# Performance work log

Hardware: AMD Instinct MI355X
Metric: run time of the kernel (lower is better)

Reference implementation:

```python
import jax, jax.numpy as jnp
import numpy as np
from jax import lax

C = 64
RED = 8
BN_EPS = 1e-5

def _conv1x1(x, W, b):
    # x: [N,C,H,W], W: [O,C] (1x1 conv kernel squeezed), b: [O]
    return jnp.einsum('nchw,oc->nohw', x, W) + b[None, :, None, None]

def _cross_attention(img, depth, Wq, bq, Wk, bk, Wv, bv, gamma):
    # img, depth: [N,C,H,W]; channel-channel attention (attn is [N,C,C])
    N, c, H, Wd = img.shape
    HW = H * Wd
    q = _conv1x1(img, Wq, bq).reshape(N, c, HW).astype(jnp.float32)
    k = _conv1x1(depth, Wk, bk).reshape(N, c, HW).astype(jnp.float32)
    v = _conv1x1(depth, Wv, bv).reshape(N, c, HW).astype(jnp.float32)
    attn = jax.nn.softmax(jnp.einsum('nci,ndi->ncd', q, k), axis=-1)  # [N,C,C]
    out = jnp.einsum('ncd,ndi->nci', attn, v).reshape(N, c, H, Wd).astype(img.dtype)
    return gamma * out + img

def _mlp(x, w1, b1, w2, b2):
    h = jax.nn.relu(x @ w1.T + b1)
    return h @ w2.T + b2

def _cbam(x, fc1_w, fc1_b, fc2_w, fc2_b, sa_w, sa_b):
    # x: [N,C,H,W]
    avg = x.mean(axis=(2, 3))          # [N,C]
    mx = x.max(axis=(2, 3))            # [N,C]
    ch = jax.nn.sigmoid(_mlp(avg, fc1_w, fc1_b, fc2_w, fc2_b)
                        + _mlp(mx, fc1_w, fc1_b, fc2_w, fc2_b))  # [N,C]
    x = x * ch[:, :, None, None]
    sp_in = jnp.stack([x.mean(axis=1), x.max(axis=1)], axis=1)   # [N,2,H,W]
    sp = lax.conv_general_dilated(sp_in, sa_w, (1, 1), 'SAME',
                                  dimension_numbers=('NCHW', 'OIHW', 'NCHW')) + sa_b[None, :, None, None]
    return x * jax.nn.sigmoid(sp)


def setup_inputs() -> dict:
    key = jax.random.key(0)
    ks = jax.random.split(key, 20)
    B, S, H, W = 2, 8, 128, 128
    s = 0.05
    d = {
        'img_feat': jax.random.normal(ks[0], (B, S, C, H, W), jnp.float32),
        'depth_feat': jax.random.normal(ks[1], (B, S, C, H, W), jnp.float32),
        # CrossAttention (shared module, used for both directions)
        'Wq': jax.random.normal(ks[2], (C, C), jnp.float32) * s,
        'bq': jax.random.normal(ks[3], (C,), jnp.float32) * s,
        'Wk': jax.random.normal(ks[4], (C, C), jnp.float32) * s,
        'bk': jax.random.normal(ks[5], (C,), jnp.float32) * s,
        'Wv': jax.random.normal(ks[6], (C, C), jnp.float32) * s,
        'bv': jax.random.normal(ks[7], (C,), jnp.float32) * s,
        'gamma': jax.random.normal(ks[8], (1,), jnp.float32) * 0.5,
        # fusion conv (3x3, 2C -> C) + BN (inference, running stats)
        'Wf': jax.random.normal(ks[9], (C, 2 * C, 3, 3), jnp.float32) * s,
        'bf': jax.random.normal(ks[10], (C,), jnp.float32) * s,
        'bn_g': jnp.ones((C,), jnp.float32),
        'bn_b': jnp.zeros((C,), jnp.float32),
        'bn_m': jax.random.normal(ks[11], (C,), jnp.float32) * s,
        'bn_v': jax.random.uniform(ks[12], (C,), jnp.float32, 0.5, 1.5),
        # CBAM channel MLP + spatial conv (7x7, 2 -> 1)
        'fc1_w': jax.random.normal(ks[13], (C // RED, C), jnp.float32) * s,
        'fc1_b': jax.random.normal(ks[14], (C // RED,), jnp.float32) * s,
        'fc2_w': jax.random.normal(ks[15], (C, C // RED), jnp.float32) * s,
        'fc2_b': jax.random.normal(ks[16], (C,), jnp.float32) * s,
        'sa_w': jax.random.normal(ks[17], (1, 2, 7, 7), jnp.float32) * s,
        'sa_b': jax.random.normal(ks[18], (1,), jnp.float32) * s,
    }
    return d


def reference(img_feat, depth_feat, Wq, bq, Wk, bk, Wv, bv, gamma,
              Wf, bf, bn_g, bn_b, bn_m, bn_v,
              fc1_w, fc1_b, fc2_w, fc2_b, sa_w, sa_b):
    B, S, c, H, W = img_feat.shape
    img = img_feat.reshape(-1, c, H, W)
    dep = depth_feat.reshape(-1, c, H, W)
    img_att = _cross_attention(img, dep, Wq, bq, Wk, bk, Wv, bv, gamma)
    dep_att = _cross_attention(dep, img, Wq, bq, Wk, bk, Wv, bv, gamma)
    fused = jnp.concatenate([img_att, dep_att], axis=1)  # [N,2C,H,W]
    fused = lax.conv_general_dilated(fused, Wf, (1, 1), 'SAME',
                                     dimension_numbers=('NCHW', 'OIHW', 'NCHW')) + bf[None, :, None, None]
    inv = bn_g * lax.rsqrt(bn_v + BN_EPS)
    fused = jax.nn.relu(fused * inv[None, :, None, None] + (bn_b - bn_m * inv)[None, :, None, None])
    fused = _cbam(fused, fc1_w, fc1_b, fc2_w, fc2_b, sa_w, sa_b)
    return fused.reshape(B, S, c, H, W)
```

## Files before the change

### kernel.cpp

```cpp
#include <hip/hip_runtime.h>
#include <math.h>


typedef __bf16 bf16_t;
typedef bf16_t bf16x8 __attribute__((ext_vector_type(8)));
typedef bf16_t bf16x4 __attribute__((ext_vector_type(4)));
typedef float  f32x4  __attribute__((ext_vector_type(4)));
typedef _Float16 f16_t;
typedef f16_t  f16x8  __attribute__((ext_vector_type(8)));

static constexpr int  CH  = 64;
static constexpr int  H   = 128;
static constexpr int  W   = 128;
static constexpr int  HW  = H * W;
static constexpr int  NI  = 16;
static constexpr int  NCK = 16;

static constexpr int W_WQ=0, W_BQ=4096, W_WK=4160, W_BK=8256, W_WV=8320, W_BV=12416,
  W_GAMMA=12480, W_WF=12481, W_BF=86209, W_BNG=86273, W_BNB=86337, W_BNM=86401,
  W_BNV=86465, W_FC1W=86529, W_FC1B=87041, W_FC2W=87049, W_FC2B=87561,
  W_SAW=87625, W_SAB=87723, W_TOTAL=87724;

static constexpr size_t OFF_GPART  = 0;
static constexpr size_t SZ_GPART   = (size_t)NI*NCK*4096*4;
static constexpr size_t OFF_SX     = OFF_GPART + SZ_GPART;
static constexpr size_t SZ_SXY     = (size_t)NI*NCK*64*4;
static constexpr size_t OFF_SY     = OFF_SX + SZ_SXY;
static constexpr size_t OFF_M1     = OFF_SY + SZ_SXY;
static constexpr size_t SZ_M       = (size_t)NI*4096*4;
static constexpr size_t OFF_M2     = OFF_M1 + SZ_M;
static constexpr size_t OFF_T1     = OFF_M2 + SZ_M;
static constexpr size_t SZ_T       = (size_t)NI*64*4;
static constexpr size_t OFF_T2     = OFF_T1 + SZ_T;
static constexpr size_t OFF_BCONST = OFF_T2 + SZ_T;
static constexpr size_t OFF_WH     = OFF_BCONST + 256;
static constexpr size_t SZ_WH      = (size_t)NI*64*9*128*2;
static constexpr size_t OFF_WINDT  = OFF_WH + SZ_WH;
static constexpr size_t SZ_WIND    = (size_t)NI*9*64*4;
static constexpr size_t OFF_IND    = OFF_WINDT + SZ_WIND;
static constexpr size_t OFF_BSUM   = OFF_IND + SZ_WIND;
static constexpr size_t SZ_BST     = (size_t)NI*64*64*4;
static constexpr size_t OFF_BMAX   = OFF_BSUM + SZ_BST;
static constexpr size_t OFF_CHS    = OFF_BMAX + SZ_BST;
static constexpr size_t OFF_SPIN   = OFF_CHS + SZ_T;
static constexpr size_t SZ_SPIN    = (size_t)NI*2*HW*4;
static constexpr size_t OFF_FLAG   = OFF_SPIN + SZ_SPIN;
static constexpr size_t OFF_WF32   = OFF_FLAG + 256;
static constexpr size_t OFF_WFT    = ((OFF_WF32 + (size_t)W_TOTAL*4 + 255) / 256) * 256;
static constexpr size_t SZ_WFT     = (size_t)9*8192*4;
static constexpr size_t OFF_P16    = ((OFF_WFT + SZ_WFT + 255) / 256) * 256;
static constexpr size_t SZ_P16     = (size_t)NI*4*HW*32*2;

__global__ __launch_bounds__(256) void k0_detect(
    const unsigned short* __restrict__ u, int* __restrict__ flag)
{
  __shared__ int bad;
  if (threadIdx.x == 0) bad = 0;
  __syncthreads();
  int local = 0;
  for (int i = threadIdx.x; i < 4096; i += 256) {
    const unsigned short v = u[2*i];
    const int e = (v >> 7) & 0xFF;
    if (e >= 0xC0) local = 1;
  }
  if (local) atomicOr(&bad, 1);
  __syncthreads();
  if (threadIdx.x == 0) flag[0] = bad;
}

struct WPack { const void* p[19]; int sz[19]; int off[19]; };

__global__ __launch_bounds__(256) void kw_convert(
    WPack wp, const int* __restrict__ flag, float* __restrict__ dst,
    float* __restrict__ WFT)
{
  const int j = blockIdx.y;
  const int i = blockIdx.x * 256 + threadIdx.x;
  if (i >= wp.sz[j]) return;
  const int f32m = flag[0];
  float v;
  if (f32m) v = ((const float*)wp.p[j])[i];
  else      v = (float)((const bf16_t*)wp.p[j])[i];
  dst[wp.off[j] + i] = v;
  if (j == 7) WFT[(i % 9) * 8192 + (i / 9)] = v;
}

__global__ __launch_bounds__(256) void kc_pack(
    const bf16_t* __restrict__ Xb, const bf16_t* __restrict__ Yb,
    const float* __restrict__ Xf, const float* __restrict__ Yf,
    const int* __restrict__ flag, f16_t* __restrict__ P16)
{
  const int lin = blockIdx.x * 256 + threadIdx.x;
  const int oct = lin & 3;
  const int p   = (lin >> 2) & 16383;
  const int s   = (lin >> 16) & 3;
  const int n   = lin >> 18;
  const int f32m = flag[0];
  const size_t nbase = (size_t)n * CH * HW;
  const int c0 = (s & 1) * 32 + oct * 8;
  const float*  Fsrc = (s < 2) ? Xf : Yf;
  const bf16_t* Bsrc = (s < 2) ? Xb : Yb;
  f16x8 h;
  #pragma unroll
  for (int j = 0; j < 8; ++j) {
    const size_t q = nbase + (size_t)(c0 + j) * HW + p;
    const float v = f32m ? Fsrc[q] : (float)Bsrc[q];
    h[j] = (f16_t)v;
  }
  *(f16x8*)(P16 + (size_t)lin * 8) = h;
}

__global__ __launch_bounds__(256) void k1_gram(
    const bf16_t* __restrict__ Xb, const bf16_t* __restrict__ Yb,
    const float* __restrict__ Xf, const float* __restrict__ Yf,
    const int* __restrict__ flag,
    float* __restrict__ Gpart, float* __restrict__ sxpart, float* __restrict__ sypart)
{
  const int chunk = blockIdx.x, n = blockIdx.y;
  const int t = threadIdx.x, lane = t & 63, wv = t >> 6;
  const int mrow = lane & 15, quad = lane >> 4;
  const int f32m = flag[0];
  const size_t nbase = (size_t)n * CH * HW;
  const int p0 = chunk * 1024 + wv * 256;

  f32x4 acc[4][4], acc2[4][4];
  #pragma unroll
  for (int i = 0; i < 4; ++i)
    #pragma unroll
    for (int j = 0; j < 4; ++j) {
      acc[i][j]  = (f32x4){0.f, 0.f, 0.f, 0.f};
      acc2[i][j] = (f32x4){0.f, 0.f, 0.f, 0.f};
    }
  float sxl[4] = {0.f,0.f,0.f,0.f}, syl[4] = {0.f,0.f,0.f,0.f};

  for (int kt = 0; kt < 8; ++kt) {
    const int pk = p0 + kt * 32 + quad * 8;
    if (f32m) {
      bf16x8 a[4], b[4], al[4], bl[4];
      #pragma unroll
      for (int mt = 0; mt < 4; ++mt) {
        const size_t ia = nbase + (size_t)(mt*16 + mrow) * HW + pk;
        float sa = 0.f, sb = 0.f;
        #pragma unroll
        for (int j = 0; j < 8; ++j) {
          const float va = Xf[ia + j];
          const bf16_t ha = (bf16_t)va;
          a[mt][j] = ha; al[mt][j] = (bf16_t)(va - (float)ha); sa += va;
          const float vb = Yf[ia + j];
          const bf16_t hb = (bf16_t)vb;
          b[mt][j] = hb; bl[mt][j] = (bf16_t)(vb - (float)hb); sb += vb;
        }
        sxl[mt] += sa; syl[mt] += sb;
      }
      #pragma unroll
      for (int mt = 0; mt < 4; ++mt)
        #pragma unroll
        for (int nt = 0; nt < 4; ++nt) {
          acc[mt][nt]  = __builtin_amdgcn_mfma_f32_16x16x32_bf16(a[mt],  b[nt],  acc[mt][nt],  0, 0, 0);
          acc2[mt][nt] = __builtin_amdgcn_mfma_f32_16x16x32_bf16(a[mt],  bl[nt], acc2[mt][nt], 0, 0, 0);
          acc2[mt][nt] = __builtin_amdgcn_mfma_f32_16x16x32_bf16(al[mt], b[nt],  acc2[mt][nt], 0, 0, 0);
        }
    } else {
      bf16x8 a[4], b[4];
      #pragma unroll
      for (int mt = 0; mt < 4; ++mt) {
        const size_t ia = nbase + (size_t)(mt*16 + mrow) * HW + pk;
        a[mt] = *(const bf16x8*)(Xb + ia);
        b[mt] = *(const bf16x8*)(Yb + ia);
        float sa = 0.f, sb = 0.f;
        #pragma unroll
        for (int j = 0; j < 8; ++j) { sa += (float)a[mt][j]; sb += (float)b[mt][j]; }
        sxl[mt] += sa; syl[mt] += sb;
      }
      #pragma unroll
      for (int mt = 0; mt < 4; ++mt)
        #pragma unroll
        for (int nt = 0; nt < 4; ++nt)
          acc[mt][nt] = __builtin_amdgcn_mfma_f32_16x16x32_bf16(a[mt], b[nt], acc[mt][nt], 0, 0, 0);
    }
  }

  #pragma unroll
  for (int mt = 0; mt < 4; ++mt) {
    sxl[mt] += __shfl_xor(sxl[mt], 16, 64); sxl[mt] += __shfl_xor(sxl[mt], 32, 64);
    syl[mt] += __shfl_xor(syl[mt], 16, 64); syl[mt] += __shfl_xor(syl[mt], 32, 64);
  }

  __shared__ float Gs[4096];
  __shared__ float sxs[64], sys[64];
  for (int w2 = 0; w2 < 4; ++w2) {
    if (wv == w2) {
      #pragma unroll
      for (int mt = 0; mt < 4; ++mt) {
        #pragma unroll
        for (int nt = 0; nt < 4; ++nt) {
          #pragma unroll
          for (int r = 0; r < 4; ++r) {
            const int c = mt*16 + quad*4 + r, d = nt*16 + mrow;
            const float val = acc[mt][nt][r] + acc2[mt][nt][r];
            if (w2 == 0) Gs[c*64 + d]  = val;
            else         Gs[c*64 + d] += val;
          }
        }
        if (quad == 0) {
          const int c = mt*16 + mrow;
          if (w2 == 0) { sxs[c] = sxl[mt];  sys[c] = syl[mt]; }
          else         { sxs[c] += sxl[mt]; sys[c] += syl[mt]; }
        }
      }
    }
    __syncthreads();
  }
  float* Gp = Gpart + ((size_t)n*NCK + chunk) * 4096;
  for (int i = t; i < 4096; i += 256) Gp[i] = Gs[i];
  if (t < 64)       sxpart[((size_t)n*NCK + chunk)*64 + t]        = sxs[t];
  else if (t < 128) sypart[((size_t)n*NCK + chunk)*64 + (t - 64)] = sys[t - 64];
}

__global__ __launch_bounds__(256, 1) void k2a_attn(
    const float* __restrict__ Gpart, const float* __restrict__ sxpart, const float* __restrict__ sypart,
    const float* __restrict__ wt,
    float* __restrict__ M1, float* __restrict__ M2,
    float* __restrict__ T1, float* __restrict__ T2)
{
  const int n = blockIdx.x, t = threadIdx.x;
  constexpr int SW = 68;
  __shared__ float Gs[4096];
  __shared__ float P1s[4096], P2s[4096];
  __shared__ float A1s[64*SW], A2s[64*SW];
  __shared__ float WQs[64*SW], WKs[64*SW], WVs[64*SW];
  __shared__ float sxs[64], sys[64], ux[64], uy[64], vx[64], vy[64];

  for (int i = t; i < 4096; i += 256) {
    const int r = i >> 6, cc = i & 63;
    WQs[r*SW + cc] = wt[W_WQ + i];
    WKs[r*SW + cc] = wt[W_WK + i];
    WVs[r*SW + cc] = wt[W_WV + i];
  }
  for (int i4 = t; i4 < 1024; i4 += 256) {
    f32x4 s = (f32x4){0.f, 0.f, 0.f, 0.f};
    for (int c2 = 0; c2 < NCK; ++c2)
      s += *(const f32x4*)(Gpart + ((size_t)n*NCK + c2)*4096 + i4*4);
    *(f32x4*)(Gs + i4*4) = s;
  }
  if (t < 64) {
    float s = 0.f; for (int c2 = 0; c2 < NCK; ++c2) s += sxpart[((size_t)n*NCK + c2)*64 + t];
    sxs[t] = s;
  } else if (t < 128) {
    const int c = t - 64;
    float s = 0.f; for (int c2 = 0; c2 < NCK; ++c2) s += sypart[((size_t)n*NCK + c2)*64 + c];
    sys[c] = s;
  }
  __syncthreads();

  {
    const int e = t & 63;
    float Greg[64], GTreg[64];
    #pragma unroll
    for (int a = 0; a < 64; ++a) Greg[a] = Gs[a*64 + e];
    #pragma unroll
    for (int a4 = 0; a4 < 16; ++a4)
      *(f32x4*)(GTreg + a4*4) = *(const f32x4*)(Gs + e*64 + a4*4);
    for (int it = 0; it < 16; ++it) {
      const int c = (t >> 6) + 4*it;
      float s1 = 0.f, s2 = 0.f;
      #pragma unroll
      for (int a4 = 0; a4 < 16; ++a4) {
        const f32x4 w4 = *(const f32x4*)(WQs + c*SW + a4*4);
        #pragma unroll
        for (int r = 0; r < 4; ++r) {
          s1 += w4[r] * Greg[a4*4 + r];
          s2 += w4[r] * GTreg[a4*4 + r];
        }
      }
      P1s[c*64 + e] = s1; P2s[c*64 + e] = s2;
    }
  }
  {
    const int which = t >> 6, c = t & 63;
    const float* Wrow = (which < 2) ? (WQs + c*SW) : (WKs + c*SW);
    const float* vecv = ((which & 1) == 0) ? sxs : sys;
    float s = 0.f;
    #pragma unroll
    for (int a = 0; a < 64; ++a) s += Wrow[a] * vecv[a];
    if      (which == 0) ux[c] = s;
    else if (which == 1) uy[c] = s;
    else if (which == 2) vx[c] = s;
    else                 vy[c] = s;
  }
  __syncthreads();

  {
    const int d = t & 63;
    float WKreg[64];
    #pragma unroll
    for (int a4 = 0; a4 < 16; ++a4)
      *(f32x4*)(WKreg + a4*4) = *(const f32x4*)(WKs + d*SW + a4*4);
    const float bkd = wt[W_BK + d];
    for (int it = 0; it < 16; ++it) {
      const int c = (t >> 6) + 4*it;
      float s1 = 0.f, s2 = 0.f;
      #pragma unroll
      for (int e4 = 0; e4 < 16; ++e4) {
        const f32x4 p1 = *(const f32x4*)(P1s + c*64 + e4*4);
        const f32x4 p2 = *(const f32x4*)(P2s + c*64 + e4*4);
        #pragma unroll
        for (int r = 0; r < 4; ++r) {
          s1 += p1[r] * WKreg[e4*4 + r];
          s2 += p2[r] * WKreg[e4*4 + r];
        }
      }
      const float bqc = wt[W_BQ + c];
      s1 += ux[c]*bkd + bqc*vy[d] + 16384.f*bqc*bkd;
      s2 += uy[c]*bkd + bqc*vx[d] + 16384.f*bqc*bkd;
      A1s[c*SW + d] = s1; A2s[c*SW + d] = s2;
    }
  }
  __syncthreads();

  if (t < 128) {
    float* R = (t < 64) ? (A1s + t*SW) : (A2s + (t - 64)*SW);
    float m = R[0];
    for (int d = 1; d < 64; ++d) m = fmaxf(m, R[d]);
    float s = 0.f;
    for (int d = 0; d < 64; ++d) { const float e2 = expf(R[d] - m); R[d] = e2; s += e2; }
    const float inv = 1.f / s;
    for (int d = 0; d < 64; ++d) R[d] *= inv;
  }
  __syncthreads();

  {
    const int e = t & 63;
    float WVreg[64];
    #pragma unroll
    for (int dd = 0; dd < 64; ++dd) WVreg[dd] = WVs[dd*SW + e];
    for (int it = 0; it < 16; ++it) {
      const int c = (t >> 6) + 4*it;
      float s1 = 0.f, s2 = 0.f;
      #pragma unroll
      for (int d4 = 0; d4 < 16; ++d4) {
        const f32x4 a1 = *(const f32x4*)(A1s + c*SW + d4*4);
        const f32x4 a2 = *(const f32x4*)(A2s + c*SW + d4*4);
        #pragma unroll
        for (int r = 0; r < 4; ++r) {
          s1 += a1[r] * WVreg[d4*4 + r];
          s2 += a2[r] * WVreg[d4*4 + r];
        }
      }
      M1[(size_t)n*4096 + c*64 + e] = s1;
      M2[(size_t)n*4096 + c*64 + e] = s2;
    }
  }
  if (t < 64) {
    float s1 = 0.f, s2 = 0.f;
    for (int d = 0; d < 64; ++d) {
      const float b = wt[W_BV + d];
      s1 += A1s[t*SW + d] * b;
      s2 += A2s[t*SW + d] * b;
    }
    T1[n*64 + t] = s1; T2[n*64 + t] = s2;
  }
}

__global__ __launch_bounds__(256) void k2b_weff(
    const float* __restrict__ wt, const float* __restrict__ WFT,
    const float* __restrict__ M1, const float* __restrict__ M2,
    const float* __restrict__ T1, const float* __restrict__ T2,
    f16_t* __restrict__ Wh, float* __restrict__ windT, float* __restrict__ bconst)
{
  const int tap = blockIdx.x, dir = blockIdx.y, n = blockIdx.z;
  const int t = threadIdx.x;
  const float g = wt[W_GAMMA];
  f16_t* Whn = Wh + (size_t)n * 64 * 9 * 128;
  const float* Mo = (dir == 0) ? (M2 + (size_t)n*4096) : (M1 + (size_t)n*4096);

  __shared__ float Wfs[8192];
  __shared__ float Ms[4096];

  for (int i4 = t; i4 < 2048; i4 += 256)
    *(f32x4*)(Wfs + i4*4) = *(const f32x4*)(WFT + (size_t)tap*8192 + i4*4);
  for (int i4 = t; i4 < 1024; i4 += 256)
    *(f32x4*)(Ms + i4*4) = *(const f32x4*)(Mo + i4*4);
  __syncthreads();

  const int e = t & 63;
  float Msreg[64];
  #pragma unroll
  for (int c = 0; c < 64; ++c) Msreg[c] = Ms[c*64 + e];
  const int coff = dir ? 0 : 64;
  const int boff = dir ? 64 : 0;
  for (int it = 0; it < 16; ++it) {
    const int o = (t >> 6) + 4*it;
    const float inv = wt[W_BNG + o] * rsqrtf(wt[W_BNV + o] + 1e-5f);
    const float base = Wfs[o*128 + boff + e];
    float s = 0.f;
    #pragma unroll
    for (int c4 = 0; c4 < 16; ++c4) {
      const f32x4 w4 = *(const f32x4*)(Wfs + o*128 + coff + c4*4);
      #pragma unroll
      for (int r = 0; r < 4; ++r) s += w4[r] * Msreg[c4*4 + r];
    }
    Whn[(o*9 + tap)*128 + dir*64 + e] = (f16_t)(inv * (base + g * s));
  }

  if (dir == 0 && t < 64) {
    const int o = t;
    const float inv = wt[W_BNG + o] * rsqrtf(wt[W_BNV + o] + 1e-5f);
    float s = 0.f;
    for (int c = 0; c < 64; ++c)
      s += wt[W_WF + (o*128 + c)*9 + tap]      * T1[n*64 + c]
         + wt[W_WF + (o*128 + 64 + c)*9 + tap] * T2[n*64 + c];
    windT[((size_t)n*9 + tap)*64 + o] = inv * g * s;
    if (tap == 0 && n == 0)
      bconst[o] = wt[W_BF + o]*inv + wt[W_BNB + o] - wt[W_BNM + o]*inv;
  }
}

__global__ __launch_bounds__(64) void k2c_ind(
    const float* __restrict__ windT, float* __restrict__ ind)
{
  const int n = blockIdx.x, o = threadIdx.x;
  float w9[9];
  #pragma unroll
  for (int tp = 0; tp < 9; ++tp) w9[tp] = windT[((size_t)n*9 + tp)*64 + o];
  #pragma unroll
  for (int yc = 0; yc < 3; ++yc) {
    const int ky0 = (yc == 0) ? 1 : 0, ky1 = (yc == 2) ? 1 : 2;
    #pragma unroll
    for (int xc = 0; xc < 3; ++xc) {
      const int kx0 = (xc == 0) ? 1 : 0, kx1 = (xc == 2) ? 1 : 2;
      float s = 0.f;
      for (int ky = ky0; ky <= ky1; ++ky)
        for (int kx = kx0; kx <= kx1; ++kx) s += w9[ky*3 + kx];
      ind[((size_t)n*9 + yc*3 + xc)*64 + o] = s;
    }
  }
}

__global__ __launch_bounds__(256) void k3_conv(
    const bf16_t* __restrict__ Xb, const bf16_t* __restrict__ Yb,
    const float* __restrict__ Xf, const float* __restrict__ Yf,
    const int* __restrict__ flag,
    const f16_t* __restrict__ Wh, const float* __restrict__ bconst,
    const float* __restrict__ ind,
    const f16_t* __restrict__ P16, const int useP16,
    bf16_t* __restrict__ fusedB, float* __restrict__ fusedF,
    float* __restrict__ bsum, float* __restrict__ bmax)
{
  __shared__ __attribute__((aligned(16))) f16_t sbuf[4][130][40];
  __shared__ float sind[576], sconst[64];
  __shared__ float ssum[4][64], smax[4][64];
  const int rp = blockIdx.x, n = blockIdx.y;
  const int t = threadIdx.x, lane = t & 63, wv = t >> 6;
  const int l15 = lane & 15, quad = lane >> 4;
  const int ly = wv >> 1, ch2 = wv & 1;
  const int f32m = flag[0];
  const size_t nbase = (size_t)n * CH * HW;
  const f16_t* __restrict__ Whn = Wh + (size_t)n * 64 * 9 * 128;

  for (int i = t; i < 576; i += 256) sind[i] = ind[(size_t)n*576 + i];
  if (t < 64) sconst[t] = bconst[t];
  {
    const int r = t >> 6, cs = (t >> 5) & 1, sl = t & 31;
    sbuf[r][cs ? 129 : 0][sl] = (f16_t)0.f;
  }

  f32x4 acc[4][4];
  #pragma unroll
  for (int i = 0; i < 4; ++i)
    #pragma unroll
    for (int j = 0; j < 4; ++j) acc[i][j] = (f32x4){0.f, 0.f, 0.f, 0.f};

  if (useP16) {
    const int oct = t & 3;
    const int sl  = t >> 2;
    const f16_t* __restrict__ PnB = P16 + (size_t)(n*4) * HW * 32;
    f16x8 h[8];

    #define K3_STAGE_LOAD(S)                                                  \
      { const f16_t* __restrict__ Pn = PnB + (size_t)(S) * HW * 32;           \
        _Pragma("unroll")                                                     \
        for (int i = 0; i < 8; ++i) {                                         \
          const int r  = i >> 1;                                              \
          const int x  = (i & 1) * 64 + sl;                                   \
          const int gy = rp*2 - 1 + r;                                        \
          f16x8 v;                                                            \
          _Pragma("unroll")                                                   \
          for (int k2 = 0; k2 < 8; ++k2) v[k2] = (f16_t)0.f;                  \
          if (gy >= 0 && gy < H)                                              \
            v = *(const f16x8*)(Pn + ((size_t)(gy*128 + x) * 32 + oct*8));    \
          h[i] = v;                                                           \
        } }
    #define K3_STAGE_WRITE()                                                  \
      { _Pragma("unroll")                                                     \
        for (int i = 0; i < 8; ++i) {                                         \
          const int r    = i >> 1;                                            \
          const int colL = (i & 1) * 64 + sl + 1;                             \
          *(f16x8*)&sbuf[r][colL][(oct ^ (colL & 3)) * 8] = h[i];             \
        } }

    K3_STAGE_LOAD(0)
    K3_STAGE_WRITE()
    for (int s = 0; s < 4; ++s) {
      if (s < 3) K3_STAGE_LOAD(s + 1)
      asm volatile("s_waitcnt lgkmcnt(0)" ::: "memory");
      __builtin_amdgcn_s_barrier();
      __builtin_amdgcn_s_setprio(1);
      #pragma unroll
      for (int tap = 0; tap < 9; ++tap) {
        const int ky = tap / 3, kx = tap % 3;
        f16x8 bfr[4];
        #pragma unroll
        for (int nt = 0; nt < 4; ++nt) {
          const int o = nt*16 + l15;
          bfr[nt] = *(const f16x8*)(Whn + ((o*9 + tap)*128 + s*32 + quad*8));
        }
        f16x8 afr[4];
        const int row = ly + ky;
        #pragma unroll
        for (int mt = 0; mt < 4; ++mt) {
          const int col = ch2*64 + mt*16 + l15 + kx;
          afr[mt] = *(const f16x8*)&sbuf[row][col][(quad ^ (col & 3)) * 8];
        }
        #pragma unroll
        for (int mt = 0; mt < 4; ++mt)
          #pragma unroll
          for (int nt = 0; nt < 4; ++nt)
            acc[mt][nt] = __builtin_amdgcn_mfma_f32_16x16x32_f16(afr[mt], bfr[nt], acc[mt][nt], 0, 0, 0);
      }
      __builtin_amdgcn_s_setprio(0);
      __builtin_amdgcn_s_barrier();
      if (s < 3) K3_STAGE_WRITE()
    }
    #undef K3_STAGE_LOAD
    #undef K3_STAGE_WRITE
  } else {
    const int cstage = t & 127, rsel = t >> 7;
    for (int s = 0; s < 4; ++s) {
      __syncthreads();
      #pragma unroll
      for (int pass = 0; pass < 2; ++pass) {
        const int r = rsel + 2*pass;
        const int gy = rp*2 - 1 + r;
        const bool valid = (gy >= 0) && (gy < H);
        const int colL = cstage + 1;
        #pragma unroll
        for (int oct = 0; oct < 4; ++oct) {
          f16x8 hh;
          #pragma unroll
          for (int j = 0; j < 8; ++j) {
            const int g = s*32 + oct*8 + j;
            float v = 0.f;
            if (valid) {
              const size_t q = nbase + (size_t)(g & 63)*HW + gy*W + cstage;
              v = (g < 64) ? (f32m ? Xf[q] : (float)Xb[q])
                           : (f32m ? Yf[q] : (float)Yb[q]);
            }
            hh[j] = (f16_t)v;
          }
          *(f16x8*)&sbuf[r][colL][(oct ^ (colL & 3)) * 8] = hh;
        }
      }
      __syncthreads();
      #pragma unroll
      for (int tap = 0; tap < 9; ++tap) {
        const int ky = tap / 3, kx = tap % 3;
        f16x8 bfr[4];
        #pragma unroll
        for (int nt = 0; nt < 4; ++nt) {
          const int o = nt*16 + l15;
          bfr[nt] = *(const f16x8*)(Whn + ((o*9 + tap)*128 + s*32 + quad*8));
        }
        f16x8 afr[4];
        const int row = ly + ky;
        #pragma unroll
        for (int mt = 0; mt < 4; ++mt) {
          const int col = ch2*64 + mt*16 + l15 + kx;
          afr[mt] = *(const f16x8*)&sbuf[row][col][(quad ^ (col & 3)) * 8];
        }
        #pragma unroll
        for (int mt = 0; mt < 4; ++mt)
          #pragma unroll
          for (int nt = 0; nt < 4; ++nt)
            acc[mt][nt] = __builtin_amdgcn_mfma_f32_16x16x32_f16(afr[mt], bfr[nt], acc[mt][nt], 0, 0, 0);
      }
    }
  }

  const int y = rp*2 + ly;
  const int yc = (y == 0) ? 0 : (y == H-1) ? 2 : 1;
  #pragma unroll
  for (int nt = 0; nt < 4; ++nt) {
    const int o = nt*16 + l15;
    const float bc = sconst[o];
    float ssm = 0.f, smx = 0.f;
    #pragma unroll
    for (int mt = 0; mt < 4; ++mt) {
      const int xb = ch2*64 + mt*16 + quad*4;
      f32x4 vals;
      #pragma unroll
      for (int r = 0; r < 4; ++r) {
        const int x = xb + r;
        const int xc = (x == 0) ? 0 : (x == W-1) ? 2 : 1;
        float v = acc[mt][nt][r] + bc + sind[(yc*3 + xc)*64 + o];
        v = fmaxf(v, 0.f);
        vals[r] = v; ssm += v; smx = fmaxf(smx, v);
      }
      const size_t off = nbase + (size_t)o*HW + y*W + xb;
      if (f32m) {
        *(f32x4*)(fusedF + off) = vals;
      } else {
        bf16x4 pv;
        #pragma unroll
        for (int r = 0; r < 4; ++r) pv[r] = (bf16_t)vals[r];
        *(bf16x4*)(fusedB + off) = pv;
      }
    }
    ssm += __shfl_xor(ssm, 16, 64); ssm += __shfl_xor(ssm, 32, 64);
    smx = fmaxf(smx, __shfl_xor(smx, 16, 64));
    smx = fmaxf(smx, __shfl_xor(smx, 32, 64));
    if (quad == 0) { ssum[wv][o] = ssm; smax[wv][o] = smx; }
  }
  __syncthreads();
  if (t < 64) {
    const float S = ssum[0][t] + ssum[1][t] + ssum[2][t] + ssum[3][t];
    const float M = fmaxf(fmaxf(smax[0][t], smax[1][t]), fmaxf(smax[2][t], smax[3][t]));
    bsum[((size_t)n*64 + rp)*64 + t] = S;
    bmax[((size_t)n*64 + rp)*64 + t] = M;
  }
}

__global__ __launch_bounds__(64) void k4_chgate(
    const float* __restrict__ bsum, const float* __restrict__ bmax,
    const float* __restrict__ wt, float* __restrict__ chout)
{
  const int n = blockIdx.x, t = threadIdx.x;
  __shared__ float avg[64], mxs[64], h1[8], h2[8];
  float S = 0.f, M = 0.f;
  for (int rp = 0; rp < 64; ++rp) {
    S += bsum[((size_t)n*64 + rp)*64 + t];
    M = fmaxf(M, bmax[((size_t)n*64 + rp)*64 + t]);
  }
  avg[t] = S * (1.f / 16384.f);
  mxs[t] = M;
  __syncthreads();
  if (t < 8) {
    float s = wt[W_FC1B + t];
    for (int c = 0; c < 64; ++c) s += wt[W_FC1W + t*64 + c] * avg[c];
    h1[t] = fmaxf(s, 0.f);
  } else if (t < 16) {
    const int r = t - 8;
    float s = wt[W_FC1B + r];
    for (int c = 0; c < 64; ++c) s += wt[W_FC1W + r*64 + c] * mxs[c];
    h2[r] = fmaxf(s, 0.f);
  }
  __syncthreads();
  float s = 2.f * wt[W_FC2B + t];
  for (int r = 0; r < 8; ++r) s += wt[W_FC2W + t*8 + r] * (h1[r] + h2[r]);
  chout[n*64 + t] = 1.f / (1.f + expf(-s));
}

__global__ __launch_bounds__(256) void k5_spin(
    const bf16_t* __restrict__ fusedB, const float* __restrict__ fusedF,
    const int* __restrict__ flag,
    const float* __restrict__ chs, float* __restrict__ spin)
{
  const int n = blockIdx.y;
  const int p0 = (blockIdx.x * 256 + threadIdx.x) * 8;
  const int f32m = flag[0];
  const size_t nbase = (size_t)n * CH * HW;
  const float* c = chs + n * 64;
  float s[8], m[8];
  #pragma unroll
  for (int k = 0; k < 8; ++k) { s[k] = 0.f; m[k] = 0.f; }
  if (f32m) {
    for (int o = 0; o < 64; ++o) {
      const float co = c[o];
      const float* q = fusedF + nbase + (size_t)o*HW + p0;
      const f32x4 a = *(const f32x4*)q;
      const f32x4 b = *(const f32x4*)(q + 4);
      #pragma unroll
      for (int k = 0; k < 4; ++k) {
        const float v0 = a[k] * co; s[k]   += v0; m[k]   = fmaxf(m[k],   v0);
        const float v1 = b[k] * co; s[4+k] += v1; m[4+k] = fmaxf(m[4+k], v1);
      }
    }
  } else {
    for (int o = 0; o < 64; ++o) {
      const float co = c[o];
      const bf16x8 a = *(const bf16x8*)(fusedB + nbase + (size_t)o*HW + p0);
      #pragma unroll
      for (int k = 0; k < 8; ++k) {
        const float v = (float)a[k] * co; s[k] += v; m[k] = fmaxf(m[k], v);
      }
    }
  }
  f32x4 o0, o1, o2, o3;
  #pragma unroll
  for (int k = 0; k < 4; ++k) {
    o0[k] = s[k]   * (1.f / 64.f);
    o1[k] = s[4+k] * (1.f / 64.f);
    o2[k] = m[k];
    o3[k] = m[4+k];
  }
  *(f32x4*)(spin + (size_t)n*2*HW + p0)          = o0;
  *(f32x4*)(spin + (size_t)n*2*HW + p0 + 4)      = o1;
  *(f32x4*)(spin + (size_t)n*2*HW + HW + p0)     = o2;
  *(f32x4*)(spin + (size_t)n*2*HW + HW + p0 + 4) = o3;
}

__global__ __launch_bounds__(256) void k6_final(
    bf16_t* __restrict__ fusedB, float* __restrict__ fusedF,
    const int* __restrict__ flag,
    const float* __restrict__ chs, const float* __restrict__ spin,
    const float* __restrict__ wt)
{
  const int n = blockIdx.y;
  const int p0 = (blockIdx.x * 256 + threadIdx.x) * 8;
  const int y = p0 >> 7, x0 = p0 & 127;
  const int f32m = flag[0];
  const float* s0 = spin + (size_t)n*2*HW;
  const float* s1 = s0 + HW;
  float acc[8];
  {
    const float sab = wt[W_SAB];
    #pragma unroll
    for (int k = 0; k < 8; ++k) acc[k] = sab;
  }
  for (int j = 0; j < 7; ++j) {
    const int yy = y + j - 3;
    if (yy < 0 || yy >= H) continue;
    const float* r0 = s0 + yy*W;
    const float* r1 = s1 + yy*W;
    float v0[14], v1[14];
    #pragma unroll
    for (int ii = 0; ii < 14; ++ii) {
      const int xx = x0 + ii - 3;
      const bool ok = (xx >= 0) && (xx < W);
      v0[ii] = ok ? r0[xx] : 0.f;
      v1[ii] = ok ? r1[xx] : 0.f;
    }
    #pragma unroll
    for (int i = 0; i < 7; ++i) {
      const float w0 = wt[W_SAW + j*7 + i];
      const float w1 = wt[W_SAW + 49 + j*7 + i];
      #pragma unroll
      for (int k = 0; k < 8; ++k)
        acc[k] += w0 * v0[i+k] + w1 * v1[i+k];
    }
  }
  float sp[8];
  #pragma unroll
  for (int k = 0; k < 8; ++k) sp[k] = 1.f / (1.f + expf(-acc[k]));
  const size_t nbase = (size_t)n * CH * HW;
  const float* c = chs + n * 64;
  if (f32m) {
    for (int o = 0; o < 64; ++o) {
      const float co = c[o];
      float* q = fusedF + nbase + (size_t)o*HW + p0;
      f32x4 a = *(f32x4*)q;
      f32x4 b = *(f32x4*)(q + 4);
      #pragma unroll
      for (int k = 0; k < 4; ++k) {
        a[k] = a[k] * co * sp[k];
        b[k] = b[k] * co * sp[4+k];
      }
      *(f32x4*)q       = a;
      *(f32x4*)(q + 4) = b;
    }
  } else {
    for (int o = 0; o < 64; ++o) {
      const float co = c[o];
      bf16_t* q = fusedB + nbase + (size_t)o*HW + p0;
      bf16x8 a = *(bf16x8*)q;
      #pragma unroll
      for (int k = 0; k < 8; ++k)
        a[k] = (bf16_t)((float)a[k] * co * sp[k]);
      *(bf16x8*)q = a;
    }
  }
}

extern "C" void kernel_launch(void* const* d_in, const int* in_sizes, int n_in,
                              void* d_out, int out_size, void* d_ws, size_t ws_size,
                              hipStream_t stream)
{
  (void)n_in; (void)out_size; (void)in_sizes;
  char* ws = (char*)d_ws;
  float*  Gpart  = (float*)(ws + OFF_GPART);
  float*  sxp    = (float*)(ws + OFF_SX);
  float*  syp    = (float*)(ws + OFF_SY);
  float*  M1     = (float*)(ws + OFF_M1);
  float*  M2     = (float*)(ws + OFF_M2);
  float*  T1     = (float*)(ws + OFF_T1);
  float*  T2     = (float*)(ws + OFF_T2);
  float*  bconst = (float*)(ws + OFF_BCONST);
  f16_t*  Wh     = (f16_t*)(ws + OFF_WH);
  float*  windT  = (float*)(ws + OFF_WINDT);
  float*  indt   = (float*)(ws + OFF_IND);
  float*  bsum   = (float*)(ws + OFF_BSUM);
  float*  bmax   = (float*)(ws + OFF_BMAX);
  float*  chs    = (float*)(ws + OFF_CHS);
  float*  spin   = (float*)(ws + OFF_SPIN);
  int*    flag   = (int*)  (ws + OFF_FLAG);
  float*  wf32   = (float*)(ws + OFF_WF32);
  float*  wft    = (float*)(ws + OFF_WFT);
  f16_t*  P16    = (f16_t*)(ws + OFF_P16);
  bf16_t* fusedB = (bf16_t*)d_out;
  float*  fusedF = (float*)d_out;

  const int useP16 = (ws_size >= OFF_P16 + SZ_P16) ? 1 : 0;

  const bf16_t* imgB = (const bf16_t*)d_in[0];
  const bf16_t* depB = (const bf16_t*)d_in[1];
  const float*  imgF = (const float*) d_in[0];
  const float*  depF = (const float*) d_in[1];

  WPack wp;
  static const int wsz[19] = {4096,64,4096,64,4096,64,1,73728,64,64,64,64,64,512,8,512,64,98,1};
  static const int woff[19] = {W_WQ,W_BQ,W_WK,W_BK,W_WV,W_BV,W_GAMMA,W_WF,W_BF,W_BNG,
                               W_BNB,W_BNM,W_BNV,W_FC1W,W_FC1B,W_FC2W,W_FC2B,W_SAW,W_SAB};
  for (int j = 0; j < 19; ++j) { wp.p[j] = d_in[2 + j]; wp.sz[j] = wsz[j]; wp.off[j] = woff[j]; }

  hipLaunchKernelGGL(k0_detect, dim3(1), dim3(256), 0, stream,
                     (const unsigned short*)d_in[0], flag);
  hipLaunchKernelGGL(kw_convert, dim3(288, 19), dim3(256), 0, stream, wp, flag, wf32, wft);
  if (useP16)
    hipLaunchKernelGGL(kc_pack, dim3(16384), dim3(256), 0, stream,
                       imgB, depB, imgF, depF, flag, P16);
  hipLaunchKernelGGL(k1_gram,  dim3(NCK, NI), dim3(256), 0, stream,
                     imgB, depB, imgF, depF, flag, Gpart, sxp, syp);
  hipLaunchKernelGGL(k2a_attn, dim3(NI), dim3(256), 0, stream,
                     Gpart, sxp, syp, wf32, M1, M2, T1, T2);
  hipLaunchKernelGGL(k2b_weff, dim3(9, 2, NI), dim3(256), 0, stream,
                     wf32, wft, M1, M2, T1, T2, Wh, windT, bconst);
  hipLaunchKernelGGL(k2c_ind,  dim3(NI), dim3(64), 0, stream, windT, indt);
  hipLaunchKernelGGL(k3_conv,  dim3(64, NI), dim3(256), 0, stream,
                     imgB, depB, imgF, depF, flag, Wh, bconst, indt,
                     P16, useP16, fusedB, fusedF, bsum, bmax);
  hipLaunchKernelGGL(k4_chgate, dim3(NI), dim3(64), 0, stream,
                     bsum, bmax, wf32, chs);
  hipLaunchKernelGGL(k5_spin,  dim3(8, NI), dim3(256), 0, stream,
                     fusedB, fusedF, flag, chs, spin);
  hipLaunchKernelGGL(k6_final, dim3(8, NI), dim3(256), 0, stream,
                     fusedB, fusedF, flag, chs, spin, wf32);
}
```

Measured before the change: 447.8 us.

## Widen conv tile to four rows per block, fuse indicator kernel, rebalance tail grids

The 3x3 conv kernel now processes four output rows per 512-thread block instead of two rows per 256-thread block. Each block stages six halo rows instead of four, which lowers redundant halo loads and halves the number of per-block partial reductions. The small k2c_ind kernel is removed, and the boundary-tap sums it produced are now computed inside the conv kernel's prologue, saving one launch. k5/k6 are relaunched with 128-thread blocks and twice as many blocks, at the cost of more LDS per block and possibly lower occupancy in the conv kernel.

```diff
diff --git a/kernel.cpp b/kernel.cpp
--- a/kernel.cpp
+++ b/kernel.cpp
@@ -416,40 +416,19 @@
   }
 }
 
-__global__ __launch_bounds__(64) void k2c_ind(
-    const float* __restrict__ windT, float* __restrict__ ind)
-{
-  const int n = blockIdx.x, o = threadIdx.x;
-  float w9[9];
-  #pragma unroll
-  for (int tp = 0; tp < 9; ++tp) w9[tp] = windT[((size_t)n*9 + tp)*64 + o];
-  #pragma unroll
-  for (int yc = 0; yc < 3; ++yc) {
-    const int ky0 = (yc == 0) ? 1 : 0, ky1 = (yc == 2) ? 1 : 2;
-    #pragma unroll
-    for (int xc = 0; xc < 3; ++xc) {
-      const int kx0 = (xc == 0) ? 1 : 0, kx1 = (xc == 2) ? 1 : 2;
-      float s = 0.f;
-      for (int ky = ky0; ky <= ky1; ++ky)
-        for (int kx = kx0; kx <= kx1; ++kx) s += w9[ky*3 + kx];
-      ind[((size_t)n*9 + yc*3 + xc)*64 + o] = s;
-    }
-  }
-}
-
-__global__ __launch_bounds__(256) void k3_conv(
+__global__ __launch_bounds__(512) void k3_conv(
     const bf16_t* __restrict__ Xb, const bf16_t* __restrict__ Yb,
     const float* __restrict__ Xf, const float* __restrict__ Yf,
     const int* __restrict__ flag,
     const f16_t* __restrict__ Wh, const float* __restrict__ bconst,
-    const float* __restrict__ ind,
+    const float* __restrict__ windT,
     const f16_t* __restrict__ P16, const int useP16,
     bf16_t* __restrict__ fusedB, float* __restrict__ fusedF,
     float* __restrict__ bsum, float* __restrict__ bmax)
 {
-  __shared__ __attribute__((aligned(16))) f16_t sbuf[4][130][40];
+  __shared__ __attribute__((aligned(16))) f16_t sbuf[6][130][40];
   __shared__ float sind[576], sconst[64];
-  __shared__ float ssum[4][64], smax[4][64];
+  __shared__ float ssum[8][64], smax[8][64];
   const int rp = blockIdx.x, n = blockIdx.y;
   const int t = threadIdx.x, lane = t & 63, wv = t >> 6;
   const int l15 = lane & 15, quad = lane >> 4;
@@ -458,9 +437,19 @@
   const size_t nbase = (size_t)n * CH * HW;
   const f16_t* __restrict__ Whn = Wh + (size_t)n * 64 * 9 * 128;
 
-  for (int i = t; i < 576; i += 256) sind[i] = ind[(size_t)n*576 + i];
+  for (int i = t; i < 576; i += 512) {
+    const int g = i >> 6, o = i & 63;
+    const int yc = g / 3, xc = g % 3;
+    const int ky0 = (yc == 0) ? 1 : 0, ky1 = (yc == 2) ? 1 : 2;
+    const int kx0 = (xc == 0) ? 1 : 0, kx1 = (xc == 2) ? 1 : 2;
+    float sv = 0.f;
+    for (int ky = ky0; ky <= ky1; ++ky)
+      for (int kx = kx0; kx <= kx1; ++kx)
+        sv += windT[((size_t)n*9 + ky*3 + kx)*64 + o];
+    sind[i] = sv;
+  }
   if (t < 64) sconst[t] = bconst[t];
-  {
+  if (t < 384) {
     const int r = t >> 6, cs = (t >> 5) & 1, sl = t & 31;
     sbuf[r][cs ? 129 : 0][sl] = (f16_t)0.f;
   }
@@ -473,17 +462,15 @@
 
   if (useP16) {
     const int oct = t & 3;
-    const int sl  = t >> 2;
+    const int x   = t >> 2;
     const f16_t* __restrict__ PnB = P16 + (size_t)(n*4) * HW * 32;
-    f16x8 h[8];
+    f16x8 h[6];
 
     #define K3_STAGE_LOAD(S)                                                  \
       { const f16_t* __restrict__ Pn = PnB + (size_t)(S) * HW * 32;           \
         _Pragma("unroll")                                                     \
-        for (int i = 0; i < 8; ++i) {                                         \
-          const int r  = i >> 1;                                              \
-          const int x  = (i & 1) * 64 + sl;                                   \
-          const int gy = rp*2 - 1 + r;                                        \
+        for (int i = 0; i < 6; ++i) {                                         \
+          const int gy = rp*4 - 1 + i;                                        \
           f16x8 v;                                                            \
           _Pragma("unroll")                                                   \
           for (int k2 = 0; k2 < 8; ++k2) v[k2] = (f16_t)0.f;                  \
@@ -492,12 +479,11 @@
           h[i] = v;                                                           \
         } }
     #define K3_STAGE_WRITE()                                                  \
-      { _Pragma("unroll")                                                     \
-        for (int i = 0; i < 8; ++i) {                                         \
-          const int r    = i >> 1;                                            \
-          const int colL = (i & 1) * 64 + sl + 1;                             \
-          *(f16x8*)&sbuf[r][colL][(oct ^ (colL & 3)) * 8] = h[i];             \
-        } }
+      { const int colL = x + 1;                                               \
+        _Pragma("unroll")                                                     \
+        for (int i = 0; i < 6; ++i)                                           \
+          *(f16x8*)&sbuf[i][colL][(oct ^ (colL & 3)) * 8] = h[i];             \
+      }
 
     K3_STAGE_LOAD(0)
     K3_STAGE_WRITE()
@@ -540,25 +526,27 @@
       __syncthreads();
       #pragma unroll
       for (int pass = 0; pass < 2; ++pass) {
-        const int r = rsel + 2*pass;
-        const int gy = rp*2 - 1 + r;
-        const bool valid = (gy >= 0) && (gy < H);
-        const int colL = cstage + 1;
-        #pragma unroll
-        for (int oct = 0; oct < 4; ++oct) {
-          f16x8 hh;
+        const int r = rsel + 4*pass;
+        if (r < 6) {
+          const int gy = rp*4 - 1 + r;
+          const bool valid = (gy >= 0) && (gy < H);
+          const int colL = cstage + 1;
           #pragma unroll
-          for (int j = 0; j < 8; ++j) {
-            const int g = s*32 + oct*8 + j;
-            float v = 0.f;
-            if (valid) {
-              const size_t q = nbase + (size_t)(g & 63)*HW + gy*W + cstage;
-              v = (g < 64) ? (f32m ? Xf[q] : (float)Xb[q])
-                           : (f32m ? Yf[q] : (float)Yb[q]);
+          for (int oct = 0; oct < 4; ++oct) {
+            f16x8 hh;
+            #pragma unroll
+            for (int j = 0; j < 8; ++j) {
+              const int g = s*32 + oct*8 + j;
+              float v = 0.f;
+              if (valid) {
+                const size_t q = nbase + (size_t)(g & 63)*HW + gy*W + cstage;
+                v = (g < 64) ? (f32m ? Xf[q] : (float)Xb[q])
+                             : (f32m ? Yf[q] : (float)Yb[q]);
+              }
+              hh[j] = (f16_t)v;
             }
-            hh[j] = (f16_t)v;
+            *(f16x8*)&sbuf[r][colL][(oct ^ (colL & 3)) * 8] = hh;
           }
-          *(f16x8*)&sbuf[r][colL][(oct ^ (colL & 3)) * 8] = hh;
         }
       }
       __syncthreads();
@@ -587,7 +575,7 @@
     }
   }
 
-  const int y = rp*2 + ly;
+  const int y = rp*4 + ly;
   const int yc = (y == 0) ? 0 : (y == H-1) ? 2 : 1;
   #pragma unroll
   for (int nt = 0; nt < 4; ++nt) {
@@ -623,10 +611,14 @@
   }
   __syncthreads();
   if (t < 64) {
-    const float S = ssum[0][t] + ssum[1][t] + ssum[2][t] + ssum[3][t];
-    const float M = fmaxf(fmaxf(smax[0][t], smax[1][t]), fmaxf(smax[2][t], smax[3][t]));
-    bsum[((size_t)n*64 + rp)*64 + t] = S;
-    bmax[((size_t)n*64 + rp)*64 + t] = M;
+    float S = 0.f, M = 0.f;
+    #pragma unroll
+    for (int w2 = 0; w2 < 8; ++w2) {
+      S += ssum[w2][t];
+      M = fmaxf(M, smax[w2][t]);
+    }
+    bsum[((size_t)n*32 + rp)*64 + t] = S;
+    bmax[((size_t)n*32 + rp)*64 + t] = M;
   }
 }
 
@@ -637,9 +629,9 @@
   const int n = blockIdx.x, t = threadIdx.x;
   __shared__ float avg[64], mxs[64], h1[8], h2[8];
   float S = 0.f, M = 0.f;
-  for (int rp = 0; rp < 64; ++rp) {
-    S += bsum[((size_t)n*64 + rp)*64 + t];
-    M = fmaxf(M, bmax[((size_t)n*64 + rp)*64 + t]);
+  for (int rp = 0; rp < 32; ++rp) {
+    S += bsum[((size_t)n*32 + rp)*64 + t];
+    M = fmaxf(M, bmax[((size_t)n*32 + rp)*64 + t]);
   }
   avg[t] = S * (1.f / 16384.f);
   mxs[t] = M;
@@ -660,13 +652,13 @@
   chout[n*64 + t] = 1.f / (1.f + expf(-s));
 }
 
-__global__ __launch_bounds__(256) void k5_spin(
+__global__ __launch_bounds__(128) void k5_spin(
     const bf16_t* __restrict__ fusedB, const float* __restrict__ fusedF,
     const int* __restrict__ flag,
     const float* __restrict__ chs, float* __restrict__ spin)
 {
   const int n = blockIdx.y;
-  const int p0 = (blockIdx.x * 256 + threadIdx.x) * 8;
+  const int p0 = (blockIdx.x * 128 + threadIdx.x) * 8;
   const int f32m = flag[0];
   const size_t nbase = (size_t)n * CH * HW;
   const float* c = chs + n * 64;
@@ -709,14 +701,14 @@
   *(f32x4*)(spin + (size_t)n*2*HW + HW + p0 + 4) = o3;
 }
 
-__global__ __launch_bounds__(256) void k6_final(
+__global__ __launch_bounds__(128) void k6_final(
     bf16_t* __restrict__ fusedB, float* __restrict__ fusedF,
     const int* __restrict__ flag,
     const float* __restrict__ chs, const float* __restrict__ spin,
     const float* __restrict__ wt)
 {
   const int n = blockIdx.y;
-  const int p0 = (blockIdx.x * 256 + threadIdx.x) * 8;
+  const int p0 = (blockIdx.x * 128 + threadIdx.x) * 8;
   const int y = p0 >> 7, x0 = p0 & 127;
   const int f32m = flag[0];
   const float* s0 = spin + (size_t)n*2*HW;
@@ -797,7 +789,6 @@
   float*  bconst = (float*)(ws + OFF_BCONST);
   f16_t*  Wh     = (f16_t*)(ws + OFF_WH);
   float*  windT  = (float*)(ws + OFF_WINDT);
-  float*  indt   = (float*)(ws + OFF_IND);
   float*  bsum   = (float*)(ws + OFF_BSUM);
   float*  bmax   = (float*)(ws + OFF_BMAX);
   float*  chs    = (float*)(ws + OFF_CHS);
@@ -834,14 +825,13 @@
                      Gpart, sxp, syp, wf32, M1, M2, T1, T2);
   hipLaunchKernelGGL(k2b_weff, dim3(9, 2, NI), dim3(256), 0, stream,
                      wf32, wft, M1, M2, T1, T2, Wh, windT, bconst);
-  hipLaunchKernelGGL(k2c_ind,  dim3(NI), dim3(64), 0, stream, windT, indt);
-  hipLaunchKernelGGL(k3_conv,  dim3(64, NI), dim3(256), 0, stream,
-                     imgB, depB, imgF, depF, flag, Wh, bconst, indt,
+  hipLaunchKernelGGL(k3_conv,  dim3(32, NI), dim3(512), 0, stream,
+                     imgB, depB, imgF, depF, flag, Wh, bconst, windT,
                      P16, useP16, fusedB, fusedF, bsum, bmax);
   hipLaunchKernelGGL(k4_chgate, dim3(NI), dim3(64), 0, stream,
                      bsum, bmax, wf32, chs);
-  hipLaunchKernelGGL(k5_spin,  dim3(8, NI), dim3(256), 0, stream,
+  hipLaunchKernelGGL(k5_spin,  dim3(16, NI), dim3(128), 0, stream,
                      fusedB, fusedF, flag, chs, spin);
-  hipLaunchKernelGGL(k6_final, dim3(8, NI), dim3(256), 0, stream,
+  hipLaunchKernelGGL(k6_final, dim3(16, NI), dim3(128), 0, stream,
                      fusedB, fusedF, flag, chs, spin, wf32);
 }
```

New measurement: 453.6 us. No clear change (+1.3%).
